# Kernel optimization log

Hardware: AMD Instinct MI355X
Metric: run time of the kernel (lower is better)

## Reference

```python
import jax, jax.numpy as jnp
import numpy as np

B, C, H, W = 16, 256, 64, 64
NH, WS = 8, 8  # num_heads, window_size
HD = C // NH   # head_dim = 32


def setup_inputs() -> dict:
    key = jax.random.key(0)
    k1, k2, k3 = jax.random.split(key, 3)
    x = jax.random.normal(k1, (B, C, H, W), dtype=jnp.float32)
    w_qkv = jax.random.normal(k2, (3 * C, C), dtype=jnp.float32) * 0.02  # 1x1 conv, no bias
    w_proj = jax.random.normal(k3, (C, C), dtype=jnp.float32) * 0.02
    return {"x": x, "w_qkv": w_qkv, "w_proj": w_proj, "shift": 1}


def _window_partition(t, ws):
    # [b,c,h,w] -> [b*(h/ws)*(w/ws), ws*ws, c]
    b, c, h, w = t.shape
    t = t.reshape(b, c, h // ws, ws, w // ws, ws)
    t = t.transpose(0, 2, 4, 3, 5, 1)
    return t.reshape(-1, ws * ws, c)


def _window_reverse(t, b, c, h, w, ws):
    t = t.reshape(b, h // ws, w // ws, ws, ws, c)
    t = t.transpose(0, 5, 1, 3, 2, 4)
    return t.reshape(b, c, h, w)


def reference(x, w_qkv, w_proj, shift):
    b, c, h, w = x.shape
    ws = min(WS, h, w)
    shift_size = ws // 2 if (shift and ws > 1 and h % ws == 0 and w % ws == 0) else 0
    if shift_size > 0:
        x = jnp.roll(x, (-shift_size, -shift_size), axis=(2, 3))
    # 1x1 conv QKV: [b,c,h,w] x [3c,c] -> [b,3c,h,w]
    qkv = jnp.einsum('bchw,oc->bohw', x, w_qkv)
    q, k, v = jnp.split(qkv, 3, axis=1)
    q_t = _window_partition(q, ws)  # [Bw, S, c], S = ws*ws
    k_t = _window_partition(k, ws)
    v_t = _window_partition(v, ws)
    bw, s, _ = q_t.shape
    # heads: [Bw, nh, S, hd]
    qh = q_t.reshape(bw, s, NH, HD).transpose(0, 2, 1, 3)
    kh = k_t.reshape(bw, s, NH, HD).transpose(0, 2, 1, 3)
    vh = v_t.reshape(bw, s, NH, HD).transpose(0, 2, 1, 3)
    scale = 1.0 / jnp.sqrt(jnp.asarray(HD, dtype=qh.dtype))
    scores = jnp.einsum('bnqd,bnkd->bnqk', qh, kh) * scale
    attn = jax.nn.softmax(scores, axis=-1)
    out = jnp.einsum('bnqk,bnkd->bnqd', attn, vh)
    out = out.transpose(0, 2, 1, 3).reshape(bw, s, c)
    out = _window_reverse(out, b, c, h, w, ws)
    if shift_size > 0:
        out = jnp.roll(out, (shift_size, shift_size), axis=(2, 3))
    return jnp.einsum('bchw,oc->bohw', out, w_proj)
```

## Files before the change

### kernel.cpp

```cpp
#include <hip/hip_runtime.h>

typedef short bf16x8 __attribute__((ext_vector_type(8)));
typedef float f32x4 __attribute__((ext_vector_type(4)));
typedef unsigned short u16;
typedef unsigned int u32;

static __device__ __forceinline__ u16 f2bf(float f) {
  u32 u = __builtin_bit_cast(u32, f);
  u32 r = (u + 0x7FFFu + ((u >> 16) & 1u)) >> 16;
  return (u16)r;
}

__global__ __launch_bounds__(256) void k_conv(
    const float* __restrict__ wqkv, const float* __restrict__ wproj,
    u16* __restrict__ wbf) {
  const int cid = blockIdx.x * 256 + threadIdx.x;
  const float* src;
  int dst;
  if (cid < 24576) {
    const int tile = cid >> 9, rem = cid & 511;
    const int k = rem >> 6, lane = rem & 63;
    src = wqkv + (size_t)(tile * 16 + (lane & 15)) * 256 + k * 32 + (lane >> 4) * 8;
    dst = cid;
  } else {
    const int pid = cid - 24576;
    const int mt = pid >> 9, rem = pid & 511;
    const int h = rem >> 6, lane = rem & 63;
    src = wproj + (size_t)(mt * 16 + (lane & 15)) * 256 + h * 32 + (lane >> 4) * 8;
    dst = 24576 + h * 1024 + mt * 64 + lane;
  }
  float4 f0 = *(const float4*)(src);
  float4 f1 = *(const float4*)(src + 4);
  ushort4 a, b;
  a.x = f2bf(f0.x); a.y = f2bf(f0.y); a.z = f2bf(f0.z); a.w = f2bf(f0.w);
  b.x = f2bf(f1.x); b.y = f2bf(f1.y); b.z = f2bf(f1.z); b.w = f2bf(f1.w);
  *(ushort4*)(wbf + (size_t)dst * 8) = a;
  *(ushort4*)(wbf + (size_t)dst * 8 + 4) = b;
}

#define QH 0
#define KH 2560
#define VTH 5120
#define PH 7424
#define LDS_TOT 16896

#define MEMF() asm volatile("" ::: "memory")
#define BAR()                        \
  do {                               \
    MEMF();                          \
    __builtin_amdgcn_s_barrier();    \
    MEMF();                          \
  } while (0)
#define WLG0() asm volatile("s_waitcnt lgkmcnt(0)" ::: "memory")

#define LOADF(FR, TI)                                              \
  do {                                                             \
    const u16* fp_ = wbf + (size_t)(TI) * 4096 + lane * 8;         \
    _Pragma("unroll") for (int k = 0; k < 8; ++k)                  \
        FR[k] = *(const bf16x8*)(fp_ + k * 512);                   \
  } while (0)

#define GEMM_TILE_F(FR, DSTB, U)                                              \
  do {                                                                        \
    f32x4 a0 = {0.f, 0.f, 0.f, 0.f}, a1 = {0.f, 0.f, 0.f, 0.f};               \
    _Pragma("unroll") for (int k = 0; k < 8; ++k) {                           \
      a0 = __builtin_amdgcn_mfma_f32_16x16x32_bf16(af0[k], FR[k], a0, 0, 0, 0);\
      a1 = __builtin_amdgcn_mfma_f32_16x16x32_bf16(af1[k], FR[k], a1, 0, 0, 0);\
    }                                                                         \
    _Pragma("unroll") for (int r = 0; r < 4; ++r) {                           \
      LDS[(DSTB) + (wp * 32 + quad * 4 + r) * 40 + (U) * 16 + l15] =          \
          f2bf(a0[r]);                                                        \
      LDS[(DSTB) + (wp * 32 + 16 + quad * 4 + r) * 40 + (U) * 16 + l15] =     \
          f2bf(a1[r]);                                                        \
    }                                                                         \
  } while (0)

#define V_TILE_F(FR, U)                                                       \
  do {                                                                        \
    f32x4 a0 = {0.f, 0.f, 0.f, 0.f}, a1 = {0.f, 0.f, 0.f, 0.f};               \
    _Pragma("unroll") for (int k = 0; k < 8; ++k) {                           \
      a0 = __builtin_amdgcn_mfma_f32_16x16x32_bf16(af0[k], FR[k], a0, 0, 0, 0);\
      a1 = __builtin_amdgcn_mfma_f32_16x16x32_bf16(af1[k], FR[k], a1, 0, 0, 0);\
    }                                                                         \
    ushort4 pk0, pk1;                                                         \
    pk0.x = f2bf(a0[0]); pk0.y = f2bf(a0[1]);                                 \
    pk0.z = f2bf(a0[2]); pk0.w = f2bf(a0[3]);                                 \
    pk1.x = f2bf(a1[0]); pk1.y = f2bf(a1[1]);                                 \
    pk1.z = f2bf(a1[2]); pk1.w = f2bf(a1[3]);                                 \
    *(ushort4*)&LDS[VTH + ((U) * 16 + l15) * 72 + wp * 32 + quad * 4] = pk0;  \
    *(ushort4*)&LDS[VTH + ((U) * 16 + l15) * 72 + wp * 32 + 16 + quad * 4] =  \
        pk1;                                                                  \
  } while (0)

__global__ __launch_bounds__(256, 2) void k_fused(
    const float* __restrict__ x, const u16* __restrict__ wbf,
    const int* __restrict__ shiftp, float* __restrict__ out) {
  __shared__ u16 LDS[LDS_TOT];
  const int blk = blockIdx.x;
  const int win = ((blk & 127) << 3) | (blk >> 7);
  const int b = win >> 6, wh = (win >> 3) & 7, ww = win & 7;
  const int off = (shiftp[0] != 0) ? 4 : 0;
  const int t = threadIdx.x;

  {
    const int slot = (blk >> 8) & 3;
    if (slot == 1) __builtin_amdgcn_s_sleep(16);
    else if (slot == 2) __builtin_amdgcn_s_sleep(32);
    else if (slot == 3) __builtin_amdgcn_s_sleep(48);
  }

  {
    u16* X = LDS;
    const int wr = t & 7;
    const int h = ((wh << 3) + wr + off) & 63;
    const int w0 = ((ww << 3) + off) & 63;
    const int w1 = ((ww << 3) + off + 4) & 63;
    const int p0 = wr << 3;
#pragma unroll
    for (int it = 0; it < 8; ++it) {
      const int c = (t >> 3) + (it << 5);
      const float* src = x + ((size_t)(b * 256 + c) * 64 + h) * 64;
      float4 v0 = *(const float4*)(src + w0);
      float4 v1 = *(const float4*)(src + w1);
      X[(p0 + 0) * 264 + c] = f2bf(v0.x);
      X[(p0 + 1) * 264 + c] = f2bf(v0.y);
      X[(p0 + 2) * 264 + c] = f2bf(v0.z);
      X[(p0 + 3) * 264 + c] = f2bf(v0.w);
      X[(p0 + 4) * 264 + c] = f2bf(v1.x);
      X[(p0 + 5) * 264 + c] = f2bf(v1.y);
      X[(p0 + 6) * 264 + c] = f2bf(v1.z);
      X[(p0 + 7) * 264 + c] = f2bf(v1.w);
    }
  }
  __syncthreads();

  const int lane = t & 63, wv = t >> 6;
  const int l15 = lane & 15, quad = lane >> 4;
  const int wp = wv >> 1, wc = wv & 1;
  const int apos0 = wv * 16 + quad * 4;

  bf16x8 af0[8], af1[8];
#pragma unroll
  for (int k = 0; k < 8; ++k) {
    af0[k] = *(const bf16x8*)&LDS[(wp * 32 + l15) * 264 + quad * 8 + k * 32];
    af1[k] =
        *(const bf16x8*)&LDS[(wp * 32 + 16 + l15) * 264 + quad * 8 + k * 32];
  }
  WLG0();
  BAR();

  f32x4 accP[8][2];
#pragma unroll
  for (int mt = 0; mt < 8; ++mt) {
    accP[mt][0] = (f32x4){0.f, 0.f, 0.f, 0.f};
    accP[mt][1] = (f32x4){0.f, 0.f, 0.f, 0.f};
  }

  const float scale = 0.17677669529663687f;
  u16* Pw = LDS + PH + wv * 1152;

#pragma unroll 1
  for (int h = 0; h < 8; ++h) {
    {
      bf16x8 fA[8], fB[8];
      const int t0 = wc ? (17 + h * 2) : (h * 2);
      const int t1 = wc ? (32 + h * 2) : (h * 2 + 1);
      const int t2 = wc ? (33 + h * 2) : (16 + h * 2);
      LOADF(fA, t0);
      LOADF(fB, t1);
      if (wc == 0) GEMM_TILE_F(fA, QH, 0); else GEMM_TILE_F(fA, KH, 1);
      LOADF(fA, t2);
      if (wc == 0) GEMM_TILE_F(fB, QH, 1); else V_TILE_F(fB, 0);
      if (wc == 0) GEMM_TILE_F(fA, KH, 0); else V_TILE_F(fA, 1);
    }
    WLG0();
    BAR();
    {
      bf16x8 aq = *(const bf16x8*)&LDS[QH + (wv * 16 + l15) * 40 + quad * 8];
      f32x4 sc[4];
#pragma unroll
      for (int nt = 0; nt < 4; ++nt) {
        bf16x8 bk = *(const bf16x8*)&LDS[KH + (nt * 16 + l15) * 40 + quad * 8];
        f32x4 z = {0.f, 0.f, 0.f, 0.f};
        sc[nt] = __builtin_amdgcn_mfma_f32_16x16x32_bf16(aq, bk, z, 0, 0, 0);
      }
#pragma unroll
      for (int r = 0; r < 4; ++r) {
        float mx = -1e30f;
#pragma unroll
        for (int nt = 0; nt < 4; ++nt) mx = fmaxf(mx, sc[nt][r]);
        mx = fmaxf(mx, __shfl_xor(mx, 1));
        mx = fmaxf(mx, __shfl_xor(mx, 2));
        mx = fmaxf(mx, __shfl_xor(mx, 4));
        mx = fmaxf(mx, __shfl_xor(mx, 8));
        float p[4], sum = 0.f;
#pragma unroll
        for (int nt = 0; nt < 4; ++nt) {
          p[nt] = __expf((sc[nt][r] - mx) * scale);
          sum += p[nt];
        }
        sum += __shfl_xor(sum, 1);
        sum += __shfl_xor(sum, 2);
        sum += __shfl_xor(sum, 4);
        sum += __shfl_xor(sum, 8);
        const float is = 1.f / sum;
#pragma unroll
        for (int nt = 0; nt < 4; ++nt)
          Pw[(quad * 4 + r) * 72 + nt * 16 + l15] = f2bf(p[nt] * is);
      }
      f32x4 oa[2];
      oa[0] = (f32x4){0.f, 0.f, 0.f, 0.f};
      oa[1] = (f32x4){0.f, 0.f, 0.f, 0.f};
#pragma unroll
      for (int kk = 0; kk < 2; ++kk) {
        bf16x8 ap = *(const bf16x8*)&Pw[l15 * 72 + kk * 32 + quad * 8];
#pragma unroll
        for (int n2 = 0; n2 < 2; ++n2) {
          bf16x8 bv = *(const bf16x8*)&LDS[VTH + (n2 * 16 + l15) * 72 +
                                           kk * 32 + quad * 8];
          oa[n2] = __builtin_amdgcn_mfma_f32_16x16x32_bf16(ap, bv, oa[n2], 0, 0, 0);
        }
      }
#pragma unroll
      for (int n2 = 0; n2 < 2; ++n2)
#pragma unroll
        for (int r = 0; r < 4; ++r)
          LDS[QH + (apos0 + r) * 40 + n2 * 16 + l15] = f2bf(oa[n2][r]);
    }
    bf16x8 pjf[8];
    {
      const u16* pp_ =
          wbf + 196608 + (size_t)h * 8192 + (size_t)wc * 4096 + lane * 8;
#pragma unroll
      for (int j = 0; j < 8; ++j) pjf[j] = *(const bf16x8*)(pp_ + j * 512);
    }
    WLG0();
    BAR();
    {
      bf16x8 bo0 = *(const bf16x8*)&LDS[QH + (wp * 32 + l15) * 40 + quad * 8];
      bf16x8 bo1 =
          *(const bf16x8*)&LDS[QH + (wp * 32 + 16 + l15) * 40 + quad * 8];
#pragma unroll
      for (int mt = 0; mt < 8; ++mt) {
        accP[mt][0] =
            __builtin_amdgcn_mfma_f32_16x16x32_bf16(pjf[mt], bo0, accP[mt][0], 0, 0, 0);
        accP[mt][1] =
            __builtin_amdgcn_mfma_f32_16x16x32_bf16(pjf[mt], bo1, accP[mt][1], 0, 0, 0);
      }
    }
    WLG0();
    BAR();
  }

#pragma unroll
  for (int i = 0; i < 2; ++i) {
    const int pos = wp * 32 + i * 16 + l15;
    const int hco = ((wh << 3) + (pos >> 3) + off) & 63;
    const int wco = ((ww << 3) + (pos & 7) + off) & 63;
#pragma unroll
    for (int mt = 0; mt < 8; ++mt)
#pragma unroll
      for (int r = 0; r < 4; ++r) {
        const int c = wc * 128 + mt * 16 + quad * 4 + r;
        out[((size_t)(b * 256 + c) << 12) + (hco << 6) + wco] = accP[mt][i][r];
      }
  }
}

extern "C" void kernel_launch(void* const* d_in, const int* in_sizes, int n_in,
                              void* d_out, int out_size, void* d_ws, size_t ws_size,
                              hipStream_t stream) {
  const float* x = (const float*)d_in[0];
  const float* wqkv = (const float*)d_in[1];
  const float* wproj = (const float*)d_in[2];
  const int* shiftp = (const int*)d_in[3];
  float* outp = (float*)d_out;
  u16* wbf = (u16*)d_ws;
  hipLaunchKernelGGL(k_conv, dim3(128), dim3(256), 0, stream, wqkv, wproj, wbf);
  hipLaunchKernelGGL(k_fused, dim3(1024), dim3(256), 0, stream, x, wbf, shiftp, outp);
}
```

Baseline: 211.7 us.

## Software-pipeline per-head QKV GEMM and projection with double-buffered LDS

Restructures the per-head loop so the QKV projection for head h+1 and the output projection for head h-1 run in the same phase as attention for head h. Double-buffered LDS regions for Q/K/V and for the attention output let a single barrier per iteration replace three. This targets barrier stalls and exposed global-load latency for weight fragments. In exchange, LDS use grows from about 33KB to 48KB per block and register pressure rises, since fA, fB and pjf are now live together, which could reduce occupancy at 2 blocks per CU.

```diff
diff --git a/kernel.cpp b/kernel.cpp
--- a/kernel.cpp
+++ b/kernel.cpp
@@ -38,11 +38,14 @@
   *(ushort4*)(wbf + (size_t)dst * 8 + 4) = b;
 }
 
-#define QH 0
-#define KH 2560
-#define VTH 5120
-#define PH 7424
-#define LDS_TOT 16896
+#define HB0 0
+#define HB1 7424
+#define KH_OFF 2560
+#define VT_OFF 5120
+#define OB0 14848
+#define OB1 17408
+#define PH 19968
+#define LDS_TOT 24576
 
 #define MEMF() asm volatile("" ::: "memory")
 #define BAR()                        \
@@ -75,7 +78,7 @@
     }                                                                         \
   } while (0)
 
-#define V_TILE_F(FR, U)                                                       \
+#define V_TILE_F(FR, VB, U)                                                   \
   do {                                                                        \
     f32x4 a0 = {0.f, 0.f, 0.f, 0.f}, a1 = {0.f, 0.f, 0.f, 0.f};               \
     _Pragma("unroll") for (int k = 0; k < 8; ++k) {                           \
@@ -87,9 +90,29 @@
     pk0.z = f2bf(a0[2]); pk0.w = f2bf(a0[3]);                                 \
     pk1.x = f2bf(a1[0]); pk1.y = f2bf(a1[1]);                                 \
     pk1.z = f2bf(a1[2]); pk1.w = f2bf(a1[3]);                                 \
-    *(ushort4*)&LDS[VTH + ((U) * 16 + l15) * 72 + wp * 32 + quad * 4] = pk0;  \
-    *(ushort4*)&LDS[VTH + ((U) * 16 + l15) * 72 + wp * 32 + 16 + quad * 4] =  \
+    *(ushort4*)&LDS[(VB) + ((U) * 16 + l15) * 72 + wp * 32 + quad * 4] = pk0; \
+    *(ushort4*)&LDS[(VB) + ((U) * 16 + l15) * 72 + wp * 32 + 16 + quad * 4] = \
         pk1;                                                                  \
+  } while (0)
+
+#define GEMM_HEAD(HH, HBD)                                                    \
+  do {                                                                        \
+    const int t2_ = wc ? (33 + (HH) * 2) : (16 + (HH) * 2);      \
+    if (wc == 0) GEMM_TILE_F(fA, (HBD), 0);                                   \
+    else GEMM_TILE_F(fA, (HBD) + KH_OFF, 1);                                  \
+    LOADF(fA, t2_);                                                           \
+    if (wc == 0) GEMM_TILE_F(fB, (HBD), 1);                                   \
+    else V_TILE_F(fB, (HBD) + VT_OFF, 0);                                     \
+    if (wc == 0) GEMM_TILE_F(fA, (HBD) + KH_OFF, 0);                          \
+    else V_TILE_F(fA, (HBD) + VT_OFF, 1);                                     \
+  } while (0)
+
+#define LOAD_AB(HH)                                                           \
+  do {                                                                        \
+    const int t0_ = wc ? (17 + (HH) * 2) : ((HH) * 2);           \
+    const int t1_ = wc ? (32 + (HH) * 2) : ((HH) * 2 + 1);       \
+    LOADF(fA, t0_);                                                           \
+    LOADF(fB, t1_);                                                           \
   } while (0)
 
 __global__ __launch_bounds__(256, 2) void k_fused(
@@ -158,29 +181,35 @@
 
   const float scale = 0.17677669529663687f;
   u16* Pw = LDS + PH + wv * 1152;
+  bf16x8 fA[8], fB[8], pjf[8];
+
+  LOAD_AB(0);
+  GEMM_HEAD(0, HB0);
+  WLG0();
+  BAR();
 
 #pragma unroll 1
   for (int h = 0; h < 8; ++h) {
+    const int HBp = (h & 1) ? HB1 : HB0;
+    const int HBn = (h & 1) ? HB0 : HB1;
+    const int OBp = (h & 1) ? OB1 : OB0;
+    const int OBq = (h & 1) ? OB0 : OB1;
+
+    if (h < 7) LOAD_AB(h + 1);
+    if (h > 0) {
+      const u16* pp_ =
+          wbf + 196608 + (size_t)(h - 1) * 8192 + (size_t)wc * 4096 + lane * 8;
+#pragma unroll
+      for (int j = 0; j < 8; ++j) pjf[j] = *(const bf16x8*)(pp_ + j * 512);
+    }
+
     {
-      bf16x8 fA[8], fB[8];
-      const int t0 = wc ? (17 + h * 2) : (h * 2);
-      const int t1 = wc ? (32 + h * 2) : (h * 2 + 1);
-      const int t2 = wc ? (33 + h * 2) : (16 + h * 2);
-      LOADF(fA, t0);
-      LOADF(fB, t1);
-      if (wc == 0) GEMM_TILE_F(fA, QH, 0); else GEMM_TILE_F(fA, KH, 1);
-      LOADF(fA, t2);
-      if (wc == 0) GEMM_TILE_F(fB, QH, 1); else V_TILE_F(fB, 0);
-      if (wc == 0) GEMM_TILE_F(fA, KH, 0); else V_TILE_F(fA, 1);
-    }
-    WLG0();
-    BAR();
-    {
-      bf16x8 aq = *(const bf16x8*)&LDS[QH + (wv * 16 + l15) * 40 + quad * 8];
+      bf16x8 aq = *(const bf16x8*)&LDS[HBp + (wv * 16 + l15) * 40 + quad * 8];
       f32x4 sc[4];
 #pragma unroll
       for (int nt = 0; nt < 4; ++nt) {
-        bf16x8 bk = *(const bf16x8*)&LDS[KH + (nt * 16 + l15) * 40 + quad * 8];
+        bf16x8 bk =
+            *(const bf16x8*)&LDS[HBp + KH_OFF + (nt * 16 + l15) * 40 + quad * 8];
         f32x4 z = {0.f, 0.f, 0.f, 0.f};
         sc[nt] = __builtin_amdgcn_mfma_f32_16x16x32_bf16(aq, bk, z, 0, 0, 0);
       }
@@ -216,7 +245,7 @@
         bf16x8 ap = *(const bf16x8*)&Pw[l15 * 72 + kk * 32 + quad * 8];
 #pragma unroll
         for (int n2 = 0; n2 < 2; ++n2) {
-          bf16x8 bv = *(const bf16x8*)&LDS[VTH + (n2 * 16 + l15) * 72 +
+          bf16x8 bv = *(const bf16x8*)&LDS[HBp + VT_OFF + (n2 * 16 + l15) * 72 +
                                            kk * 32 + quad * 8];
           oa[n2] = __builtin_amdgcn_mfma_f32_16x16x32_bf16(ap, bv, oa[n2], 0, 0, 0);
         }
@@ -225,21 +254,15 @@
       for (int n2 = 0; n2 < 2; ++n2)
 #pragma unroll
         for (int r = 0; r < 4; ++r)
-          LDS[QH + (apos0 + r) * 40 + n2 * 16 + l15] = f2bf(oa[n2][r]);
-    }
-    bf16x8 pjf[8];
-    {
-      const u16* pp_ =
-          wbf + 196608 + (size_t)h * 8192 + (size_t)wc * 4096 + lane * 8;
-#pragma unroll
-      for (int j = 0; j < 8; ++j) pjf[j] = *(const bf16x8*)(pp_ + j * 512);
-    }
-    WLG0();
-    BAR();
-    {
-      bf16x8 bo0 = *(const bf16x8*)&LDS[QH + (wp * 32 + l15) * 40 + quad * 8];
+          LDS[OBp + (apos0 + r) * 40 + n2 * 16 + l15] = f2bf(oa[n2][r]);
+    }
+
+    if (h < 7) GEMM_HEAD(h + 1, HBn);
+
+    if (h > 0) {
+      bf16x8 bo0 = *(const bf16x8*)&LDS[OBq + (wp * 32 + l15) * 40 + quad * 8];
       bf16x8 bo1 =
-          *(const bf16x8*)&LDS[QH + (wp * 32 + 16 + l15) * 40 + quad * 8];
+          *(const bf16x8*)&LDS[OBq + (wp * 32 + 16 + l15) * 40 + quad * 8];
 #pragma unroll
       for (int mt = 0; mt < 8; ++mt) {
         accP[mt][0] =
@@ -248,8 +271,26 @@
             __builtin_amdgcn_mfma_f32_16x16x32_bf16(pjf[mt], bo1, accP[mt][1], 0, 0, 0);
       }
     }
+
     WLG0();
     BAR();
+  }
+
+  {
+    const u16* pp_ =
+        wbf + 196608 + (size_t)7 * 8192 + (size_t)wc * 4096 + lane * 8;
+#pragma unroll
+    for (int j = 0; j < 8; ++j) pjf[j] = *(const bf16x8*)(pp_ + j * 512);
+    bf16x8 bo0 = *(const bf16x8*)&LDS[OB1 + (wp * 32 + l15) * 40 + quad * 8];
+    bf16x8 bo1 =
+        *(const bf16x8*)&LDS[OB1 + (wp * 32 + 16 + l15) * 40 + quad * 8];
+#pragma unroll
+    for (int mt = 0; mt < 8; ++mt) {
+      accP[mt][0] =
+          __builtin_amdgcn_mfma_f32_16x16x32_bf16(pjf[mt], bo0, accP[mt][0], 0, 0, 0);
+      accP[mt][1] =
+          __builtin_amdgcn_mfma_f32_16x16x32_bf16(pjf[mt], bo1, accP[mt][1], 0, 0, 0);
+    }
   }
 
 #pragma unroll
```

New measurement: 246.3 us. 16.3% more time.

## Split output projection into separate kernel and prefetch next head's QKV weights

Applied to the files above, without the earlier changes.

The fused kernel no longer runs the output projection inside its per-head loop. It writes the bf16 attention output for each window to a global workspace buffer, and a new k_proj kernel then runs the projection GEMM over 8 windows per block, storing the fp32 output rows. The fused kernel also loads the next head's QKV weight fragments right after the barrier, so they overlap the attention math. This removes one barrier per head, the accumulator register pressure, and the per-window projection weight reloads. In exchange it adds a global round trip of the attention output (about 32 MB each way) and an extra kernel launch.

```diff
diff --git a/kernel.cpp b/kernel.cpp
--- a/kernel.cpp
+++ b/kernel.cpp
@@ -43,6 +43,7 @@
 #define VTH 5120
 #define PH 7424
 #define LDS_TOT 16896
+#define OBUF_OFF 262144
 
 #define MEMF() asm volatile("" ::: "memory")
 #define BAR()                        \
@@ -92,9 +93,29 @@
         pk1;                                                                  \
   } while (0)
 
+#define GEMM_HEAD(HH)                                                         \
+  do {                                                                        \
+    const int t2_ = wc ? (33 + (HH) * 2) : (16 + (HH) * 2);      \
+    if (wc == 0) GEMM_TILE_F(fA, QH, 0);                                      \
+    else GEMM_TILE_F(fA, KH, 1);                                              \
+    LOADF(fA, t2_);                                                           \
+    if (wc == 0) GEMM_TILE_F(fB, QH, 1);                                      \
+    else V_TILE_F(fB, 0);                                                     \
+    if (wc == 0) GEMM_TILE_F(fA, KH, 0);                                      \
+    else V_TILE_F(fA, 1);                                                     \
+  } while (0)
+
+#define LOAD_AB(HH)                                                           \
+  do {                                                                        \
+    const int t0_ = wc ? (17 + (HH) * 2) : ((HH) * 2);           \
+    const int t1_ = wc ? (32 + (HH) * 2) : ((HH) * 2 + 1);       \
+    LOADF(fA, t0_);                                                           \
+    LOADF(fB, t1_);                                                           \
+  } while (0)
+
 __global__ __launch_bounds__(256, 2) void k_fused(
     const float* __restrict__ x, const u16* __restrict__ wbf,
-    const int* __restrict__ shiftp, float* __restrict__ out) {
+    const int* __restrict__ shiftp, u16* __restrict__ obuf) {
   __shared__ u16 LDS[LDS_TOT];
   const int blk = blockIdx.x;
   const int win = ((blk & 127) << 3) | (blk >> 7);
@@ -149,32 +170,18 @@
   WLG0();
   BAR();
 
-  f32x4 accP[8][2];
-#pragma unroll
-  for (int mt = 0; mt < 8; ++mt) {
-    accP[mt][0] = (f32x4){0.f, 0.f, 0.f, 0.f};
-    accP[mt][1] = (f32x4){0.f, 0.f, 0.f, 0.f};
-  }
-
   const float scale = 0.17677669529663687f;
   u16* Pw = LDS + PH + wv * 1152;
-
+  u16* Ow = obuf + (size_t)win * 16384;
+  bf16x8 fA[8], fB[8];
+
+  LOAD_AB(0);
 #pragma unroll 1
   for (int h = 0; h < 8; ++h) {
-    {
-      bf16x8 fA[8], fB[8];
-      const int t0 = wc ? (17 + h * 2) : (h * 2);
-      const int t1 = wc ? (32 + h * 2) : (h * 2 + 1);
-      const int t2 = wc ? (33 + h * 2) : (16 + h * 2);
-      LOADF(fA, t0);
-      LOADF(fB, t1);
-      if (wc == 0) GEMM_TILE_F(fA, QH, 0); else GEMM_TILE_F(fA, KH, 1);
-      LOADF(fA, t2);
-      if (wc == 0) GEMM_TILE_F(fB, QH, 1); else V_TILE_F(fB, 0);
-      if (wc == 0) GEMM_TILE_F(fA, KH, 0); else V_TILE_F(fA, 1);
-    }
+    GEMM_HEAD(h);
     WLG0();
     BAR();
+    if (h < 7) LOAD_AB(h + 1);
     {
       bf16x8 aq = *(const bf16x8*)&LDS[QH + (wv * 16 + l15) * 40 + quad * 8];
       f32x4 sc[4];
@@ -225,43 +232,59 @@
       for (int n2 = 0; n2 < 2; ++n2)
 #pragma unroll
         for (int r = 0; r < 4; ++r)
-          LDS[QH + (apos0 + r) * 40 + n2 * 16 + l15] = f2bf(oa[n2][r]);
-    }
-    bf16x8 pjf[8];
-    {
-      const u16* pp_ =
-          wbf + 196608 + (size_t)h * 8192 + (size_t)wc * 4096 + lane * 8;
-#pragma unroll
-      for (int j = 0; j < 8; ++j) pjf[j] = *(const bf16x8*)(pp_ + j * 512);
+          Ow[(size_t)(apos0 + r) * 256 + h * 32 + n2 * 16 + l15] =
+              f2bf(oa[n2][r]);
     }
     WLG0();
     BAR();
-    {
-      bf16x8 bo0 = *(const bf16x8*)&LDS[QH + (wp * 32 + l15) * 40 + quad * 8];
-      bf16x8 bo1 =
-          *(const bf16x8*)&LDS[QH + (wp * 32 + 16 + l15) * 40 + quad * 8];
-#pragma unroll
-      for (int mt = 0; mt < 8; ++mt) {
-        accP[mt][0] =
-            __builtin_amdgcn_mfma_f32_16x16x32_bf16(pjf[mt], bo0, accP[mt][0], 0, 0, 0);
-        accP[mt][1] =
-            __builtin_amdgcn_mfma_f32_16x16x32_bf16(pjf[mt], bo1, accP[mt][1], 0, 0, 0);
-      }
-    }
-    WLG0();
-    BAR();
-  }
-
-#pragma unroll
-  for (int i = 0; i < 2; ++i) {
-    const int pos = wp * 32 + i * 16 + l15;
+  }
+}
+
+__global__ __launch_bounds__(512, 1) void k_proj(
+    const u16* __restrict__ wbf, const int* __restrict__ shiftp,
+    float* __restrict__ out) {
+  const int blk = blockIdx.x;
+  const int b = blk >> 4, wh = (blk >> 1) & 7, ch = blk & 1;
+  const int off = (shiftp[0] != 0) ? 4 : 0;
+  const int t = threadIdx.x, lane = t & 63, wv = t >> 6;
+  const int l15 = lane & 15, quad = lane >> 4;
+  const int win = b * 64 + wh * 8 + wv;
+  const u16* Ob = wbf + OBUF_OFF + (size_t)win * 16384;
+
+  f32x4 accP[8][4];
+#pragma unroll
+  for (int mt = 0; mt < 8; ++mt)
+#pragma unroll
+    for (int i = 0; i < 4; ++i) accP[mt][i] = (f32x4){0.f, 0.f, 0.f, 0.f};
+
+#pragma unroll 1
+  for (int h = 0; h < 8; ++h) {
+    bf16x8 aw[8], bo[4];
+    const u16* pp_ =
+        wbf + 196608 + (size_t)h * 8192 + (size_t)ch * 4096 + lane * 8;
+#pragma unroll
+    for (int mt = 0; mt < 8; ++mt) aw[mt] = *(const bf16x8*)(pp_ + mt * 512);
+#pragma unroll
+    for (int i = 0; i < 4; ++i)
+      bo[i] = *(const bf16x8*)&Ob[(size_t)(i * 16 + l15) * 256 + h * 32 + quad * 8];
+#pragma unroll
+    for (int mt = 0; mt < 8; ++mt)
+#pragma unroll
+      for (int i = 0; i < 4; ++i)
+        accP[mt][i] =
+            __builtin_amdgcn_mfma_f32_16x16x32_bf16(aw[mt], bo[i], accP[mt][i], 0, 0, 0);
+  }
+
+#pragma unroll
+  for (int i = 0; i < 4; ++i) {
+    const int pos = i * 16 + l15;
     const int hco = ((wh << 3) + (pos >> 3) + off) & 63;
-    const int wco = ((ww << 3) + (pos & 7) + off) & 63;
+    const int wco = ((wv << 3) + (pos & 7) + off) & 63;
 #pragma unroll
     for (int mt = 0; mt < 8; ++mt)
 #pragma unroll
       for (int r = 0; r < 4; ++r) {
-        const int c = wc * 128 + mt * 16 + quad * 4 + r;
+        const int c = ch * 128 + mt * 16 + quad * 4 + r;
         out[((size_t)(b * 256 + c) << 12) + (hco << 6) + wco] = accP[mt][i][r];
       }
   }
@@ -277,5 +300,7 @@
   float* outp = (float*)d_out;
   u16* wbf = (u16*)d_ws;
   hipLaunchKernelGGL(k_conv, dim3(128), dim3(256), 0, stream, wqkv, wproj, wbf);
-  hipLaunchKernelGGL(k_fused, dim3(1024), dim3(256), 0, stream, x, wbf, shiftp, outp);
-}
+  hipLaunchKernelGGL(k_fused, dim3(1024), dim3(256), 0, stream, x, wbf, shiftp,
+                     wbf + OBUF_OFF);
+  hipLaunchKernelGGL(k_proj, dim3(256), dim3(512), 0, stream, wbf, shiftp, outp);
+}
```

Result: slower. 243.5 us (+15.0%).
